# Kernel optimization log

Measured on AMD Instinct MI355X. Metric: run time of the kernel, lower is better.

## Reference

```python
import jax, jax.numpy as jnp
import numpy as np

FEATURE_LEN = 64
DIM_ATOM = 256
DIM_GRAPH = 256
NUM_NEI = 32
B = 2048          # reactions / graphs in batch
ATOMS = 30        # atoms per molecule graph
N = B * ATOMS     # total nodes
E = 4 * N         # total edges
NMOL = 100000     # knowledge-graph molecule table size
S = 2             # molecules per reaction side (len(id_list))


def setup_inputs() -> dict:
    key = jax.random.key(0)
    ks = jax.random.split(key, 16)
    xavier = lambda k, shape: (jax.random.normal(k, shape, jnp.float32)
                               * np.sqrt(2.0 / (shape[0] + shape[-1])))
    return {
        "node_feat": jax.random.randint(ks[0], (N, 4), 0, FEATURE_LEN, jnp.int32),
        "edge_src": jax.random.randint(ks[1], (E,), 0, N, jnp.int32),
        "edge_dst": jax.random.randint(ks[2], (E,), 0, N, jnp.int32),
        "graph_ids": jnp.repeat(jnp.arange(B, dtype=jnp.int32), ATOMS),
        "id_list": jax.random.randint(ks[3], (S, B), 0, NMOL, jnp.int32),
        "id_list_target": jax.random.randint(ks[4], (S, B), 0, NMOL, jnp.int32),
        "all_mfea": (jax.random.uniform(ks[5], (NMOL, 40)) < 0.3).astype(jnp.float32),
        "neighbor_matrix": jax.random.randint(ks[6], (NMOL, NUM_NEI), 0, NMOL, jnp.int32),
        "W0": xavier(ks[7], (FEATURE_LEN, DIM_ATOM)),
        "b0": jnp.zeros((DIM_ATOM,), jnp.float32),
        "W1": xavier(ks[8], (DIM_ATOM, DIM_ATOM)),
        "b1": jnp.zeros((DIM_ATOM,), jnp.float32),
        "fea_emb": xavier(ks[9], (40, DIM_GRAPH)),
        "att_w": xavier(ks[10], (DIM_GRAPH, 1)),
        "att_b": jnp.zeros((1,), jnp.float32),
        "crosscl_w": xavier(ks[11], (DIM_GRAPH, DIM_ATOM)),
        "crosscl_b": jnp.zeros((DIM_ATOM,), jnp.float32),
    }


def reference(node_feat, edge_src, edge_dst, graph_ids, id_list, id_list_target,
              all_mfea, neighbor_matrix,
              W0, b0, W1, b1, fea_emb, att_w, att_b, crosscl_w, crosscl_b):
    n = node_feat.shape[0]
    # --- atom-level GCN (DGL GraphConv, norm='both') ---
    h = jax.nn.one_hot(node_feat, FEATURE_LEN, dtype=jnp.float32).sum(axis=1)  # [N, F]
    ones_e = jnp.ones((edge_src.shape[0],), jnp.float32)
    deg_out = jnp.clip(jax.ops.segment_sum(ones_e, edge_src, n), 1.0)
    deg_in = jnp.clip(jax.ops.segment_sum(ones_e, edge_dst, n), 1.0)
    norm_src = deg_out[:, None] ** -0.5
    norm_dst = deg_in[:, None] ** -0.5

    def gcn(x, W, b, act):
        m = (x * norm_src)[edge_src]                        # gather along edges
        agg = jax.ops.segment_sum(m, edge_dst, n)           # scatter-add
        z = (agg * norm_dst) @ W + b
        return act(z)

    h = gcn(h, W0, b0, jax.nn.relu)
    h = gcn(h, W1, b1, lambda z: z)
    # factor computed via python float() in torch -> detached constant
    factor = np.sqrt(DIM_ATOM).astype(np.float32) / jax.lax.stop_gradient(
        jnp.mean(jnp.linalg.norm(h, axis=1)))
    h = h * factor
    mol_atom_embedding = jax.ops.segment_sum(h, graph_ids, B)  # SumPooling [B, D]

    # --- reaction-level KG aggregation ---
    src_emb = jnp.einsum('sbf,fg->sbg', all_mfea[id_list], fea_emb)         # [S,B,G]
    tgt_emb = jnp.einsum('sbf,fg->sbg', all_mfea[id_list_target], fea_emb)  # [S,B,G]
    source_re = src_emb.mean(axis=0)   # 1/len * sum
    target_re = tgt_emb.mean(axis=0)

    item_emb = src_emb                                       # [S,B,G]
    nei_idx = neighbor_matrix[id_list]                       # [S,B,K]
    nei_emb = jnp.einsum('sbkf,fg->sbkg', all_mfea[nei_idx], fea_emb)  # [S,B,K,G]

    target_embedding = source_re + target_re                 # [B,G]
    score_nei = item_emb[:, :, None, :] * nei_emb * target_embedding[None, :, None, :]
    logits = score_nei @ att_w + att_b                       # [S,B,K,1]
    score_att = jax.nn.softmax(logits, axis=2)
    nei_agg = jnp.sum(score_att * nei_emb, axis=2)           # [S,B,G]

    mol_reaction_embedding = (item_emb + nei_agg).mean(axis=0)  # [B,G]
    mol_x_embedding = mol_reaction_embedding @ crosscl_w + crosscl_b
    mol_embedding = jnp.concatenate([mol_atom_embedding, mol_reaction_embedding], axis=1)
    return mol_embedding, mol_atom_embedding, mol_x_embedding
```

## Files before the change

### kernel.cpp

```cpp
#include <hip/hip_runtime.h>
#include <math.h>

#define N_NODES 61440
#define N_EDGES 245760
#define BATCH   2048
#define ATOMS   30
#define F_LEN   64
#define DIM     256
#define NUM_NEI 32
#define MF      40
#define ECAP    512
#define CHUNK   64

typedef __attribute__((ext_vector_type(8))) short s8v;
typedef __attribute__((ext_vector_type(4))) float f4v;
typedef __attribute__((address_space(3))) unsigned lds_u32;
typedef const __attribute__((address_space(1))) unsigned glb_u32;

__device__ __forceinline__ unsigned short f2bf(float x) {
    union { float f; unsigned u; } c; c.f = x;
    unsigned r = (c.u + 0x7FFFu + ((c.u >> 16) & 1u)) >> 16;
    return (unsigned short)r;
}
__device__ __forceinline__ float bf2f(unsigned short u) {
    union { unsigned u; float f; } c; c.u = ((unsigned)u) << 16;
    return c.f;
}

__global__ void k_deg(const int* __restrict__ esrc, const int* __restrict__ edst,
                      int* deg_out, int* deg_in) {
    int e = blockIdx.x * 256 + threadIdx.x;
    if (e < N_EDGES) {
        atomicAdd(&deg_out[esrc[e]], 1);
        atomicAdd(&deg_in[edst[e]], 1);
    }
}

__global__ void k_alloc(const int* __restrict__ deg_in, int* row_start, int* cursor,
                        int* counter) {
    int t = threadIdx.x;
    int n = blockIdx.x * 256 + t;
    int lane = t & 63;
    int d = deg_in[n];
    int p = d;
#pragma unroll
    for (int o = 1; o < 64; o <<= 1) { int v = __shfl_up(p, o, 64); if (lane >= o) p += v; }
    int base = 0;
    if (lane == 63) base = atomicAdd(counter, p);
    base = __shfl(base, 63, 64);
    int v = base + p - d;
    row_start[n] = v;
    cursor[n] = v;
}

__global__ void k_csr_fill(const int* __restrict__ esrc, const int* __restrict__ edst,
                           int* cursor, int* csr_src) {
    int e = blockIdx.x * 256 + threadIdx.x;
    if (e < N_EDGES) {
        int p = atomicAdd(&cursor[edst[e]], 1);
        csr_src[p] = esrc[e];
    }
}

__global__ void k_prepw(const float* __restrict__ W0, const float* __restrict__ W1,
                        unsigned short* w0bt, unsigned short* w1bt) {
    int n = blockIdx.x, k = threadIdx.x;
    w1bt[(size_t)n * 256 + k] = f2bf(W1[(size_t)k * 256 + n]);
    if (k < 64) w0bt[(size_t)n * 64 + k] = f2bf(W0[(size_t)k * 256 + n]);
}

__global__ __launch_bounds__(256) void k_gcn0(
    const int* __restrict__ nf, const int* __restrict__ row_start,
    const int* __restrict__ csr_src, const int* __restrict__ deg_in,
    const int* __restrict__ deg_out, const unsigned short* __restrict__ w0bt,
    const float* __restrict__ b0, unsigned short* __restrict__ h1b) {
    __shared__ float la0[32 * 68];
    __shared__ int4  enf[ECAP];
    __shared__ float ens[ECAP];
    __shared__ int   rs[33];
    __shared__ float lnd[32], lns[32];
    __shared__ float b0c[256];
    int n0 = blockIdx.x * 32;
    int t = threadIdx.x;
    if (t < 32) rs[t] = row_start[n0 + t];
    if (t == 0) rs[32] = row_start[n0 + 31] + deg_in[n0 + 31];
    if (t < 32) {
        lnd[t] = rsqrtf((float)max(deg_in[n0 + t], 1));
        lns[t] = rsqrtf((float)max(deg_out[n0 + t], 1));
    }
    b0c[t] = b0[t];
    __syncthreads();
    int beg0 = rs[0];
    int tot = rs[32] - beg0; if (tot > ECAP) tot = ECAP;
    for (int e = t; e < tot; e += 256) {
        int s = csr_src[beg0 + e];
        enf[e] = ((const int4*)nf)[s];
        ens[e] = rsqrtf((float)max(deg_out[s], 1));
    }
    __syncthreads();
    {
        int row = t >> 3, kc = (t & 7) * 8;
        float a[8];
#pragma unroll
        for (int j = 0; j < 8; j++) a[j] = 0.f;
        int lo = rs[row] - beg0, hi = rs[row + 1] - beg0;
        if (hi > tot) hi = tot;
        for (int e = lo; e < hi; e++) {
            int4 f = enf[e]; float w = ens[e];
#pragma unroll
            for (int j = 0; j < 8; j++) {
                int k = kc + j;
                a[j] += w * (float)((f.x == k) + (f.y == k) + (f.z == k) + (f.w == k));
            }
        }
#pragma unroll
        for (int j = 0; j < 8; j++) la0[row * 68 + kc + j] = a[j];
    }
    __syncthreads();
    int lane = t & 63, wv = t >> 6;
    int ln = lane & 15, lg = lane >> 4;
    f4v acc[2][4];
#pragma unroll
    for (int mi = 0; mi < 2; mi++)
#pragma unroll
        for (int ni = 0; ni < 4; ni++) acc[mi][ni] = (f4v)0.f;
#pragma unroll
    for (int kst = 0; kst < 2; kst++) {
        s8v afr[2];
#pragma unroll
        for (int mi = 0; mi < 2; mi++) {
            const float* p = &la0[(mi * 16 + ln) * 68 + kst * 32 + lg * 8];
            f4v lo = *(const f4v*)p;
            f4v hi = *(const f4v*)(p + 4);
            s8v a;
#pragma unroll
            for (int j = 0; j < 4; j++) { a[j] = (short)f2bf(lo[j]); a[4 + j] = (short)f2bf(hi[j]); }
            afr[mi] = a;
        }
#pragma unroll
        for (int ni = 0; ni < 4; ni++) {
            int n = wv * 64 + ni * 16 + ln;
            s8v b = *(const s8v*)&w0bt[(size_t)n * 64 + kst * 32 + lg * 8];
            acc[0][ni] = __builtin_amdgcn_mfma_f32_16x16x32_bf16(afr[0], b, acc[0][ni], 0, 0, 0);
            acc[1][ni] = __builtin_amdgcn_mfma_f32_16x16x32_bf16(afr[1], b, acc[1][ni], 0, 0, 0);
        }
    }
#pragma unroll
    for (int mi = 0; mi < 2; mi++)
#pragma unroll
        for (int ni = 0; ni < 4; ni++) {
            int n = wv * 64 + ni * 16 + ln;
            float bb = b0c[n];
#pragma unroll
            for (int r = 0; r < 4; r++) {
                int m = mi * 16 + lg * 4 + r;
                float z = acc[mi][ni][r] * lnd[m] + bb;
                z = fmaxf(z, 0.f) * lns[m];
                h1b[(size_t)(n0 + m) * 256 + n] = f2bf(z);
            }
        }
}

__global__ __launch_bounds__(256) void k_gcn1(
    const unsigned short* __restrict__ h1b, const int* __restrict__ row_start,
    const int* __restrict__ csr_src, const int* __restrict__ deg_in,
    const unsigned short* __restrict__ w1bt, const float* __restrict__ b1,
    unsigned short* __restrict__ h2b, float* __restrict__ partial) {
    __shared__ unsigned short stage[CHUNK * 256];
    __shared__ unsigned short lab[32 * 264];
    __shared__ int   ecache[ECAP];
    __shared__ int   rs[33];
    __shared__ float lnd[32];
    __shared__ float b1c[256];
    __shared__ float nsq[32];
    int n0 = blockIdx.x * 32;
    int t = threadIdx.x;
    int lane = t & 63, wv = t >> 6;
    if (t < 32) rs[t] = row_start[n0 + t];
    if (t == 0) rs[32] = row_start[n0 + 31] + deg_in[n0 + 31];
    if (t < 32) {
        lnd[t] = rsqrtf((float)max(deg_in[n0 + t], 1));
        nsq[t] = 0.f;
    }
    b1c[t] = b1[t];
    __syncthreads();
    int beg0 = rs[0];
    int tot = rs[32] - beg0; if (tot > ECAP) tot = ECAP;
    for (int e = t; e < tot; e += 256) ecache[e] = csr_src[beg0 + e];
    __syncthreads();
    int gr = t >> 5;
    int gc = (t & 31) * 8;
    int lo[4], hi[4];
#pragma unroll
    for (int r = 0; r < 4; r++) {
        int i = gr + r * 8;
        lo[r] = rs[i] - beg0;
        int h = rs[i + 1] - beg0; if (h > tot) h = tot;
        hi[r] = h;
    }
    float a[4][8];
#pragma unroll
    for (int r = 0; r < 4; r++)
#pragma unroll
        for (int j = 0; j < 8; j++) a[r][j] = 0.f;
    int lhalf = (lane >> 5) & 1;
    for (int c0 = 0; c0 < tot; c0 += CHUNK) {
        int nch = min(CHUNK, tot - c0);
        int npair = (nch + 1) >> 1;
        for (int p = wv; p < npair; p += 4) {
            int e = c0 + 2 * p + lhalf;
            int ecl = min(e, tot - 1);
            int sv = ecache[ecl];
            const unsigned short* src = h1b + (size_t)sv * 256 + (lane & 31) * 8;
            __builtin_amdgcn_global_load_lds((glb_u32*)src,
                                             (lds_u32*)&stage[(size_t)(2 * p) * 256],
                                             16, 0, 0);
        }
        asm volatile("s_waitcnt vmcnt(0)" ::: "memory");
        __syncthreads();
#pragma unroll
        for (int r = 0; r < 4; r++) {
            int es = max(lo[r], c0) - c0;
            int ee = min(hi[r], c0 + nch) - c0;
            for (int e = es; e < ee; e++) {
                s8v v = *(const s8v*)&stage[e * 256 + gc];
#pragma unroll
                for (int j = 0; j < 8; j++) a[r][j] += bf2f((unsigned short)v[j]);
            }
        }
        __syncthreads();
    }
#pragma unroll
    for (int r = 0; r < 4; r++) {
        int i = gr + r * 8;
        s8v ov;
#pragma unroll
        for (int j = 0; j < 8; j++) ov[j] = (short)f2bf(a[r][j]);
        *(s8v*)&lab[i * 264 + gc] = ov;
    }
    __syncthreads();
    int ln = lane & 15, lg = lane >> 4;
    f4v acc[2][4];
#pragma unroll
    for (int mi = 0; mi < 2; mi++)
#pragma unroll
        for (int ni = 0; ni < 4; ni++) acc[mi][ni] = (f4v)0.f;
#pragma unroll 2
    for (int kst = 0; kst < 8; kst++) {
        s8v afr[2];
#pragma unroll
        for (int mi = 0; mi < 2; mi++)
            afr[mi] = *(const s8v*)&lab[(mi * 16 + ln) * 264 + kst * 32 + lg * 8];
#pragma unroll
        for (int ni = 0; ni < 4; ni++) {
            int n = wv * 64 + ni * 16 + ln;
            s8v b = *(const s8v*)&w1bt[(size_t)n * 256 + kst * 32 + lg * 8];
            acc[0][ni] = __builtin_amdgcn_mfma_f32_16x16x32_bf16(afr[0], b, acc[0][ni], 0, 0, 0);
            acc[1][ni] = __builtin_amdgcn_mfma_f32_16x16x32_bf16(afr[1], b, acc[1][ni], 0, 0, 0);
        }
    }
    float sm[2][4];
#pragma unroll
    for (int mi = 0; mi < 2; mi++)
#pragma unroll
        for (int r = 0; r < 4; r++) sm[mi][r] = 0.f;
#pragma unroll
    for (int mi = 0; mi < 2; mi++)
#pragma unroll
        for (int ni = 0; ni < 4; ni++) {
            int n = wv * 64 + ni * 16 + ln;
            float bb = b1c[n];
#pragma unroll
            for (int r = 0; r < 4; r++) {
                int m = mi * 16 + lg * 4 + r;
                float z = acc[mi][ni][r] * lnd[m] + bb;
                h2b[(size_t)(n0 + m) * 256 + n] = f2bf(z);
                sm[mi][r] += z * z;
            }
        }
#pragma unroll
    for (int mi = 0; mi < 2; mi++)
#pragma unroll
        for (int r = 0; r < 4; r++) {
            float v = sm[mi][r];
            v += __shfl_xor(v, 1);
            v += __shfl_xor(v, 2);
            v += __shfl_xor(v, 4);
            v += __shfl_xor(v, 8);
            if (ln == 0) atomicAdd(&nsq[mi * 16 + lg * 4 + r], v);
        }
    __syncthreads();
    if (t < 32) atomicAdd(&partial[(n0 + t) & 1023], sqrtf(nsq[t]));
}

__global__ void k_normfin(const float* __restrict__ partial, float* factor) {
    __shared__ float red[256];
    int t = threadIdx.x;
    float s = partial[t] + partial[t + 256] + partial[t + 512] + partial[t + 768];
    red[t] = s;
    __syncthreads();
    for (int o = 128; o; o >>= 1) {
        if (t < o) red[t] += red[t + o];
        __syncthreads();
    }
    if (t == 0) factor[0] = 16.0f / (red[0] / (float)N_NODES);
}

__global__ __launch_bounds__(256) void k_rxn(
    const int* __restrict__ id_list, const int* __restrict__ id_list_t,
    const int* __restrict__ neimat, const float* __restrict__ mfea,
    const float* __restrict__ fea_emb, const float* __restrict__ att_w,
    const float* __restrict__ att_b, const float* __restrict__ crosscl_w,
    const float* __restrict__ crosscl_b, const unsigned short* __restrict__ h2b,
    const float* __restrict__ factor, float* __restrict__ out) {
    __shared__ float com[MF];
    __shared__ float mitem[MF];
    __shared__ float u[DIM];
    __shared__ float nm[NUM_NEI * MF];
    __shared__ float vv[MF];
    __shared__ float aw[NUM_NEI];
    __shared__ float mre[DIM];
    int b = blockIdx.x;
    int t = threadIdx.x;
    int wv = t >> 6, lane = t & 63;
    float pv = 0.f;
    for (int a = 0; a < ATOMS; a++) pv += bf2f(h2b[(size_t)(b * ATOMS + a) * DIM + t]);
    pv *= factor[0];
    out[(size_t)b * 512 + t] = pv;
    out[(size_t)BATCH * 512 + (size_t)b * DIM + t] = pv;
    if (t < MF) {
        int i0 = id_list[b], i1 = id_list[BATCH + b];
        int j0 = id_list_t[b], j1 = id_list_t[BATCH + b];
        com[t] = 0.5f * (mfea[(size_t)i0 * MF + t] + mfea[(size_t)i1 * MF + t])
               + 0.5f * (mfea[(size_t)j0 * MF + t] + mfea[(size_t)j1 * MF + t]);
    }
    __syncthreads();
    float tg = 0.f;
    for (int f = 0; f < MF; f++) tg += com[f] * fea_emb[f * DIM + t];
    float awt = att_w[t];
    float msum = 0.f;
    for (int s = 0; s < 2; s++) {
        int id = id_list[s * BATCH + b];
        __syncthreads();
        if (t < MF) mitem[t] = mfea[(size_t)id * MF + t];
        for (int i = t; i < NUM_NEI * MF; i += 256) {
            int k = i / MF, f = i - k * MF;
            int nid = neimat[(size_t)id * NUM_NEI + k];
            nm[i] = mfea[(size_t)nid * MF + f];
        }
        __syncthreads();
        float item = 0.f;
        for (int f = 0; f < MF; f++) item += mitem[f] * fea_emb[f * DIM + t];
        u[t] = item * tg * awt;
        __syncthreads();
        for (int i = 0; i < 5; i++) {
            int f = wv + 8 * i;
            float p = 0.f;
#pragma unroll
            for (int j = 0; j < 4; j++) p += u[lane + 64 * j] * fea_emb[f * DIM + lane + 64 * j];
#pragma unroll
            for (int off = 32; off; off >>= 1) p += __shfl_down(p, off, 64);
            if (lane == 0) vv[f] = p;
        }
        __syncthreads();
        if (wv == 0) {
            float lg = -1e30f;
            if (lane < NUM_NEI) {
                lg = att_b[0];
                for (int f = 0; f < MF; f++) lg += nm[lane * MF + f] * vv[f];
            }
            float m = lg;
#pragma unroll
            for (int off = 16; off; off >>= 1) m = fmaxf(m, __shfl_xor(m, off, 32));
            float e = (lane < NUM_NEI) ? __expf(lg - m) : 0.f;
            float ssum = e;
#pragma unroll
            for (int off = 16; off; off >>= 1) ssum += __shfl_xor(ssum, off, 32);
            if (lane < NUM_NEI) aw[lane] = e / ssum;
        }
        __syncthreads();
        if (t < MF) {
            float w = 0.f;
            for (int k = 0; k < NUM_NEI; k++) w += aw[k] * nm[k * MF + t];
            vv[t] = w;
        }
        __syncthreads();
        float na = 0.f;
        for (int f = 0; f < MF; f++) na += vv[f] * fea_emb[f * DIM + t];
        msum += item + na;
    }
    float m = 0.5f * msum;
    out[(size_t)b * 512 + DIM + t] = m;
    mre[t] = m;
    __syncthreads();
    float acc = crosscl_b[t];
    for (int uu = 0; uu < DIM; uu++) acc += mre[uu] * crosscl_w[uu * DIM + t];
    out[(size_t)BATCH * 768 + (size_t)b * DIM + t] = acc;
}

extern "C" void kernel_launch(void* const* d_in, const int* in_sizes, int n_in,
                              void* d_out, int out_size, void* d_ws, size_t ws_size,
                              hipStream_t stream) {
    const int*   node_feat = (const int*)d_in[0];
    const int*   edge_src  = (const int*)d_in[1];
    const int*   edge_dst  = (const int*)d_in[2];
    const int*   id_list   = (const int*)d_in[4];
    const int*   id_list_t = (const int*)d_in[5];
    const float* all_mfea  = (const float*)d_in[6];
    const int*   neimat    = (const int*)d_in[7];
    const float* W0        = (const float*)d_in[8];
    const float* b0        = (const float*)d_in[9];
    const float* W1        = (const float*)d_in[10];
    const float* b1        = (const float*)d_in[11];
    const float* fea_emb   = (const float*)d_in[12];
    const float* att_w     = (const float*)d_in[13];
    const float* att_b     = (const float*)d_in[14];
    const float* crosscl_w = (const float*)d_in[15];
    const float* crosscl_b = (const float*)d_in[16];
    float* out = (float*)d_out;

    char* ws = (char*)d_ws;
    char* zbase = ws;
    int*   deg_out   = (int*)ws;            ws += (size_t)N_NODES * 4;
    int*   deg_in    = (int*)ws;            ws += (size_t)N_NODES * 4;
    float* partial   = (float*)ws;          ws += 1024 * 4;
    float* factor    = (float*)ws;
    int*   counter   = (int*)(ws + 8);      ws += 256;
    size_t zbytes = (size_t)(ws - zbase);
    int*   row_start = (int*)ws;            ws += (size_t)N_NODES * 4;
    int*   cursor    = (int*)ws;            ws += (size_t)N_NODES * 4;
    int*   csr_srcb  = (int*)ws;            ws += (size_t)N_EDGES * 4;
    unsigned short* w0bt = (unsigned short*)ws; ws += (size_t)256 * 64 * 2;
    unsigned short* w1bt = (unsigned short*)ws; ws += (size_t)256 * 256 * 2;
    unsigned short* h1b  = (unsigned short*)ws; ws += (size_t)N_NODES * DIM * 2;
    unsigned short* h2b  = (unsigned short*)ws; ws += (size_t)N_NODES * DIM * 2;

    hipMemsetAsync(zbase, 0, zbytes, stream);

    k_deg<<<(N_EDGES + 255) / 256, 256, 0, stream>>>(edge_src, edge_dst, deg_out, deg_in);
    k_alloc<<<N_NODES / 256, 256, 0, stream>>>(deg_in, row_start, cursor, counter);
    k_csr_fill<<<(N_EDGES + 255) / 256, 256, 0, stream>>>(edge_src, edge_dst, cursor, csr_srcb);
    k_prepw<<<256, 256, 0, stream>>>(W0, W1, w0bt, w1bt);

    k_gcn0<<<N_NODES / 32, 256, 0, stream>>>(node_feat, row_start, csr_srcb, deg_in,
                                             deg_out, w0bt, b0, h1b);
    k_gcn1<<<N_NODES / 32, 256, 0, stream>>>(h1b, row_start, csr_srcb, deg_in,
                                             w1bt, b1, h2b, partial);
    k_normfin<<<1, 256, 0, stream>>>(partial, factor);
    k_rxn<<<BATCH, 256, 0, stream>>>(id_list, id_list_t, neimat, all_mfea, fea_emb,
                                     att_w, att_b, crosscl_w, crosscl_b, h2b,
                                     factor, out);
}
```

Before: 191.0 us.

## Double-buffer gcn1 neighbor gather, tile weight transpose, vectorize KG neighbor loads

The gcn1 neighbor gather now uses two 32-edge LDS buffers, so loads for the next chunk are issued before the current chunk is summed. It waits with a partial vmcnt and uses raw s_barrier instead of a full drain each chunk. The separate lab buffer now aliases the stage buffer to cut LDS use, and launch bounds request 4 blocks per CU. The weight transpose uses a 64x64 shared-memory tile across 20 blocks for coalesced reads and writes, and the KG neighbor feature gather loads float4 instead of scalars. Risks include hazards from reusing the stage buffer as lab and register pressure under the tighter launch bounds.

```diff
diff --git a/kernel.cpp b/kernel.cpp
--- a/kernel.cpp
+++ b/kernel.cpp
@@ -10,7 +10,7 @@
 #define NUM_NEI 32
 #define MF      40
 #define ECAP    512
-#define CHUNK   64
+#define CH      32
 
 typedef __attribute__((ext_vector_type(8))) short s8v;
 typedef __attribute__((ext_vector_type(4))) float f4v;
@@ -62,11 +62,40 @@
     }
 }
 
-__global__ void k_prepw(const float* __restrict__ W0, const float* __restrict__ W1,
-                        unsigned short* w0bt, unsigned short* w1bt) {
-    int n = blockIdx.x, k = threadIdx.x;
-    w1bt[(size_t)n * 256 + k] = f2bf(W1[(size_t)k * 256 + n]);
-    if (k < 64) w0bt[(size_t)n * 64 + k] = f2bf(W0[(size_t)k * 256 + n]);
+__global__ __launch_bounds__(256) void k_prepw(
+    const float* __restrict__ W0, const float* __restrict__ W1,
+    unsigned short* __restrict__ w0bt, unsigned short* __restrict__ w1bt) {
+    __shared__ float tile[64][65];
+    int bi = blockIdx.x;
+    int t = threadIdx.x;
+    int c = t & 63, rq = t >> 6;
+    if (bi < 16) {
+        int tr = bi >> 2, tc = bi & 3;
+#pragma unroll 4
+        for (int pass = 0; pass < 16; pass++) {
+            int r = rq + 4 * pass;
+            tile[r][c] = W1[(size_t)(tr * 64 + r) * 256 + tc * 64 + c];
+        }
+        __syncthreads();
+#pragma unroll 4
+        for (int pass = 0; pass < 16; pass++) {
+            int nr = rq + 4 * pass;
+            w1bt[(size_t)(tc * 64 + nr) * 256 + tr * 64 + c] = f2bf(tile[c][nr]);
+        }
+    } else {
+        int tb = bi - 16;
+#pragma unroll 4
+        for (int pass = 0; pass < 16; pass++) {
+            int r = rq + 4 * pass;
+            tile[r][c] = W0[(size_t)r * 256 + tb * 64 + c];
+        }
+        __syncthreads();
+#pragma unroll 4
+        for (int pass = 0; pass < 16; pass++) {
+            int nr = rq + 4 * pass;
+            w0bt[(size_t)(tb * 64 + nr) * 64 + c] = f2bf(tile[c][nr]);
+        }
+    }
 }
 
 __global__ __launch_bounds__(256) void k_gcn0(
@@ -161,18 +190,18 @@
         }
 }
 
-__global__ __launch_bounds__(256) void k_gcn1(
+__global__ __launch_bounds__(256, 4) void k_gcn1(
     const unsigned short* __restrict__ h1b, const int* __restrict__ row_start,
     const int* __restrict__ csr_src, const int* __restrict__ deg_in,
     const unsigned short* __restrict__ w1bt, const float* __restrict__ b1,
     unsigned short* __restrict__ h2b, float* __restrict__ partial) {
-    __shared__ unsigned short stage[CHUNK * 256];
-    __shared__ unsigned short lab[32 * 264];
+    __shared__ unsigned short stage[2 * CH * 256];
     __shared__ int   ecache[ECAP];
     __shared__ int   rs[33];
     __shared__ float lnd[32];
     __shared__ float b1c[256];
     __shared__ float nsq[32];
+    unsigned short* lab = stage;
     int n0 = blockIdx.x * 32;
     int t = threadIdx.x;
     int lane = t & 63, wv = t >> 6;
@@ -188,6 +217,7 @@
     int tot = rs[32] - beg0; if (tot > ECAP) tot = ECAP;
     for (int e = t; e < tot; e += 256) ecache[e] = csr_src[beg0 + e];
     __syncthreads();
+
     int gr = t >> 5;
     int gc = (t & 31) * 8;
     int lo[4], hi[4];
@@ -203,33 +233,50 @@
     for (int r = 0; r < 4; r++)
 #pragma unroll
         for (int j = 0; j < 8; j++) a[r][j] = 0.f;
-    int lhalf = (lane >> 5) & 1;
-    for (int c0 = 0; c0 < tot; c0 += CHUNK) {
-        int nch = min(CHUNK, tot - c0);
-        int npair = (nch + 1) >> 1;
-        for (int p = wv; p < npair; p += 4) {
-            int e = c0 + 2 * p + lhalf;
-            int ecl = min(e, tot - 1);
-            int sv = ecache[ecl];
-            const unsigned short* src = h1b + (size_t)sv * 256 + (lane & 31) * 8;
-            __builtin_amdgcn_global_load_lds((glb_u32*)src,
-                                             (lds_u32*)&stage[(size_t)(2 * p) * 256],
-                                             16, 0, 0);
-        }
-        asm volatile("s_waitcnt vmcnt(0)" ::: "memory");
-        __syncthreads();
+
+    int lhalf = lane >> 5;
+    int colo = (lane & 31) * 8;
+    int nc = (tot + CH - 1) >> 5;
+#define ISSUE(c)                                                                   \
+    {                                                                              \
+        int base_ = (c) << 5;                                                      \
+        unsigned short* sb_ = stage + ((c) & 1) * (CH * 256);                      \
+        _Pragma("unroll")                                                          \
+        for (int pp = 0; pp < 4; ++pp) {                                           \
+            int p_ = wv + pp * 4;                                                  \
+            int e_ = base_ + 2 * p_ + lhalf;                                       \
+            int sv_ = ecache[min(e_, tot - 1)];                                    \
+            __builtin_amdgcn_global_load_lds(                                      \
+                (glb_u32*)(h1b + (size_t)sv_ * 256 + colo),                        \
+                (lds_u32*)(sb_ + 2 * p_ * 256), 16, 0, 0);                         \
+        }                                                                          \
+    }
+    if (nc > 0) ISSUE(0);
+    for (int c = 0; c < nc; ++c) {
+        if (c + 1 < nc) {
+            ISSUE(c + 1);
+            asm volatile("s_waitcnt vmcnt(4)" ::: "memory");
+        } else {
+            asm volatile("s_waitcnt vmcnt(0)" ::: "memory");
+        }
+        __builtin_amdgcn_sched_barrier(0);
+        __builtin_amdgcn_s_barrier();
+        int c0 = c << 5;
+        int nch = min(CH, tot - c0);
+        const unsigned short* sb = stage + (c & 1) * (CH * 256);
 #pragma unroll
         for (int r = 0; r < 4; r++) {
-            int es = max(lo[r], c0) - c0;
-            int ee = min(hi[r], c0 + nch) - c0;
+            int es = max(lo[r] - c0, 0);
+            int ee = min(hi[r] - c0, nch);
             for (int e = es; e < ee; e++) {
-                s8v v = *(const s8v*)&stage[e * 256 + gc];
+                s8v v = *(const s8v*)&sb[e * 256 + gc];
 #pragma unroll
                 for (int j = 0; j < 8; j++) a[r][j] += bf2f((unsigned short)v[j]);
             }
         }
-        __syncthreads();
-    }
+        __builtin_amdgcn_s_barrier();
+    }
+#undef ISSUE
 #pragma unroll
     for (int r = 0; r < 4; r++) {
         int i = gr + r * 8;
@@ -343,10 +390,10 @@
         int id = id_list[s * BATCH + b];
         __syncthreads();
         if (t < MF) mitem[t] = mfea[(size_t)id * MF + t];
-        for (int i = t; i < NUM_NEI * MF; i += 256) {
-            int k = i / MF, f = i - k * MF;
+        for (int i = t; i < NUM_NEI * 10; i += 256) {
+            int k = i / 10, q = i - k * 10;
             int nid = neimat[(size_t)id * NUM_NEI + k];
-            nm[i] = mfea[(size_t)nid * MF + f];
+            *(float4*)&nm[k * MF + q * 4] = *(const float4*)&mfea[(size_t)nid * MF + q * 4];
         }
         __syncthreads();
         float item = 0.f;
@@ -440,7 +487,7 @@
     k_deg<<<(N_EDGES + 255) / 256, 256, 0, stream>>>(edge_src, edge_dst, deg_out, deg_in);
     k_alloc<<<N_NODES / 256, 256, 0, stream>>>(deg_in, row_start, cursor, counter);
     k_csr_fill<<<(N_EDGES + 255) / 256, 256, 0, stream>>>(edge_src, edge_dst, cursor, csr_srcb);
-    k_prepw<<<256, 256, 0, stream>>>(W0, W1, w0bt, w1bt);
+    k_prepw<<<20, 256, 0, stream>>>(W0, W1, w0bt, w1bt);
 
     k_gcn0<<<N_NODES / 32, 256, 0, stream>>>(node_feat, row_start, csr_srcb, deg_in,
                                              deg_out, w0bt, b0, h1b);
```

Result: faster. 179.6 us (-6.0%).
